# Kernel optimization log

Measured on AMD Instinct MI355X. Metric: run time of the kernel, lower is better.

## Reference

```python
import jax, jax.numpy as jnp
import numpy as np

N_NODES = 100000
N_EDGES = 3200000
D_IN = 128
D_OUT = 128
LN_EPS = 1e-5


def setup_inputs() -> dict:
    key = jax.random.key(0)
    k1, k2, k3, k4 = jax.random.split(key, 4)
    x = jax.random.normal(k1, (N_NODES, D_IN), dtype=jnp.float32)
    edge_index = jax.random.randint(k2, (2, N_EDGES), 0, N_NODES, dtype=jnp.int64)
    # GCNConv weight (glorot-ish scale) and bias
    W = jax.random.normal(k3, (D_IN, D_OUT), dtype=jnp.float32) / np.sqrt(D_IN)
    b = jnp.zeros((D_OUT,), dtype=jnp.float32)
    # LayerNorm params
    gamma = jnp.ones((D_OUT,), dtype=jnp.float32)
    beta = jnp.zeros((D_OUT,), dtype=jnp.float32)
    return {"x": x, "edge_index": edge_index, "W": W, "b": b, "gamma": gamma, "beta": beta}


def reference(x, edge_index, W, b, gamma, beta):
    # GCNConv: add self-loops, symmetric degree normalization, aggregate, add bias.
    N = x.shape[0]
    self_loops = jnp.arange(N, dtype=edge_index.dtype)
    row = jnp.concatenate([edge_index[0], self_loops])  # destination
    col = jnp.concatenate([edge_index[1], self_loops])  # source
    deg = jax.ops.segment_sum(jnp.ones(row.shape[0], x.dtype), row, num_segments=N)
    dinv = jnp.where(deg > 0, jax.lax.rsqrt(deg), 0.0)
    norm = dinv[row] * dinv[col]                         # [E+N]
    xw = x @ W                                           # [N, D_OUT]
    msg = norm[:, None] * xw[col]                        # gather + scale [E+N, D_OUT]
    agg = jax.ops.segment_sum(msg, row, num_segments=N) + b  # scatter-add
    # LayerNorm over feature dim
    mu = jnp.mean(agg, axis=-1, keepdims=True)
    var = jnp.mean(jnp.square(agg - mu), axis=-1, keepdims=True)
    h = (agg - mu) * jax.lax.rsqrt(var + LN_EPS) * gamma + beta
    # ReLU; Dropout is identity in eval mode
    return jax.nn.relu(h)
```

## Files before the change

kernel.cpp:

```cpp
#include <hip/hip_runtime.h>

#define N_NODES 100000
#define N_EDGES 3200000
#define D 128
#define NB 782
#define BCAP 5120
#define STAGE 16

typedef __attribute__((ext_vector_type(8))) short bf16x8;
typedef __attribute__((ext_vector_type(4))) float f32x4;

__device__ __forceinline__ float bf2f(unsigned short u) {
  return __uint_as_float(((unsigned)u) << 16);
}
__device__ __forceinline__ unsigned short f2bf(float f) {
  unsigned u = __float_as_uint(f);
  u += 0x7FFF + ((u >> 16) & 1);
  return (unsigned short)(u >> 16);
}

__global__ void detect_kernel(const int* __restrict__ ei32, int* __restrict__ flag) {
  __shared__ int anynz;
  if (threadIdx.x == 0) anynz = 0;
  __syncthreads();
  int v = 0;
  for (int i = threadIdx.x; i < 2048; i += 256) v |= ei32[2 * i + 1];
  if (v) atomicOr(&anynz, 1);
  __syncthreads();
  if (threadIdx.x == 0) *flag = (anynz == 0) ? 1 : 0;
}

__global__ void zero_kernel(int* __restrict__ p, int n) {
  int i = blockIdx.x * blockDim.x + threadIdx.x;
  if (i < n) p[i] = 0;
}

__global__ void prep_w_kernel(const float* __restrict__ W, unsigned short* __restrict__ wTg) {
  int t = threadIdx.x;
  int c = t >> 1, h = t & 1;
  for (int k0 = h * 64; k0 < h * 64 + 64; k0 += 8) {
    unsigned short tmp[8];
#pragma unroll
    for (int j = 0; j < 8; j++) tmp[j] = f2bf(W[(k0 + j) * D + c]);
    *(uint4*)(wTg + c * D + k0) = *(uint4*)tmp;
  }
}

__global__ __launch_bounds__(256) void partition_kernel(const void* __restrict__ edges,
                                                        const int* __restrict__ flag,
                                                        int* __restrict__ gcur,
                                                        unsigned int* __restrict__ bstore) {
  __shared__ unsigned int stage[NB][STAGE];
  __shared__ int scnt[NB];
  const bool is64 = (*flag != 0);
  for (int i = threadIdx.x; i < NB; i += 256) scnt[i] = 0;
  __syncthreads();
  int gstride = gridDim.x * blockDim.x;
  for (int base = blockIdx.x * blockDim.x; base < N_EDGES; base += gstride) {
    int e = base + threadIdx.x;
    if (e < N_EDGES) {
      int r, c;
      if (is64) {
        r = (int)((const long long*)edges)[e];
        c = (int)((const long long*)edges)[N_EDGES + e];
      } else {
        r = ((const int*)edges)[e];
        c = ((const int*)edges)[N_EDGES + e];
      }
      int b = r >> 7;
      unsigned ent = ((unsigned)(r & 127) << 17) | (unsigned)c;
      int pos = atomicAdd(&scnt[b], 1);
      if (pos < STAGE) {
        stage[b][pos] = ent;
      } else {
        int gp = atomicAdd(&gcur[b], 1);
        if (gp < BCAP) bstore[(size_t)b * BCAP + gp] = ent;
      }
    }
    __syncthreads();
    for (int b = threadIdx.x; b < NB; b += 256) {
      if (scnt[b] >= STAGE) {
        int gp = atomicAdd(&gcur[b], STAGE);
        if (gp + STAGE <= BCAP) {
          uint4* dst = (uint4*)&bstore[(size_t)b * BCAP + gp];
          uint4* src = (uint4*)&stage[b][0];
          dst[0] = src[0];
          dst[1] = src[1];
          dst[2] = src[2];
          dst[3] = src[3];
        } else {
          for (int k = 0; k < STAGE; k++)
            if (gp + k < BCAP) bstore[(size_t)b * BCAP + gp + k] = stage[b][k];
        }
        scnt[b] = 0;
      }
    }
    __syncthreads();
  }
  for (int b = threadIdx.x; b < NB; b += 256) {
    int n = scnt[b];
    if (n > STAGE) n = STAGE;
    if (n > 0) {
      int gp = atomicAdd(&gcur[b], n);
      for (int k = 0; k < n; k++)
        if (gp + k < BCAP) bstore[(size_t)b * BCAP + gp + k] = stage[b][k];
    }
  }
}

__global__ __launch_bounds__(256) void bucket_kernel(const int* __restrict__ gcur,
                                                     unsigned int* __restrict__ bstore,
                                                     int* __restrict__ cnt,
                                                     int* __restrict__ start,
                                                     float* __restrict__ dinv) {
  __shared__ unsigned int ent[BCAP];
  __shared__ int lcnt[128];
  __shared__ int s[128];
  __shared__ int loffs[128];
  int b = blockIdx.x, tid = threadIdx.x;
  size_t base = (size_t)b * BCAP;
  int m = gcur[b];
  if (m > BCAP) m = BCAP;
  int nodes = N_NODES - b * 128;
  if (nodes > 128) nodes = 128;

  for (int i = tid; i < m; i += 256) ent[i] = bstore[base + i];
  if (tid < 128) lcnt[tid] = 0;
  __syncthreads();
  for (int i = tid; i < m; i += 256) atomicAdd(&lcnt[ent[i] >> 17], 1);
  __syncthreads();
  if (tid < 128) s[tid] = lcnt[tid];
  __syncthreads();
#pragma unroll
  for (int off = 1; off < 128; off <<= 1) {
    int v = (tid < 128 && tid >= off) ? s[tid - off] : 0;
    __syncthreads();
    if (tid < 128) s[tid] += v;
    __syncthreads();
  }
  if (tid < nodes) {
    int st = (tid == 0) ? 0 : s[tid - 1];
    int node = b * 128 + tid;
    start[node] = (int)base + st;
    cnt[node] = lcnt[tid];
    dinv[node] = rsqrtf((float)(lcnt[tid] + 1));
    loffs[tid] = st;
  }
  __syncthreads();
  for (int i = tid; i < m; i += 256) {
    unsigned u = ent[i];
    int lr = u >> 17;
    int pos = atomicAdd(&loffs[lr], 1);
    bstore[base + pos] = u & 0x1FFFF;
  }
}

__global__ __launch_bounds__(256) void gemm_mfma_kernel(const float* __restrict__ x,
                                                        const unsigned short* __restrict__ wTg,
                                                        const float* __restrict__ dinv,
                                                        unsigned short* __restrict__ y) {
  __shared__ unsigned short xs[64 * 136];
  __shared__ unsigned short wls[128 * 136];
  int tid = threadIdx.x;
  int row0 = blockIdx.x * 64;
  {
    int c = tid >> 1, h = tid & 1;
    const uint4* src = (const uint4*)(wTg + c * D + h * 64);
    uint4* dst = (uint4*)(wls + c * 136 + h * 64);
#pragma unroll
    for (int i = 0; i < 8; i++) dst[i] = src[i];
  }
  {
    int rx = tid >> 2, q = tid & 3;
    int r = row0 + rx;
    if (r > N_NODES - 1) r = N_NODES - 1;
    const float4* src = (const float4*)(x + (size_t)r * D + q * 32);
    uint4* dst = (uint4*)(xs + rx * 136 + q * 32);
#pragma unroll
    for (int i = 0; i < 4; i++) {
      float4 fa = src[2 * i], fb = src[2 * i + 1];
      uint4 p;
      p.x = (unsigned)f2bf(fa.x) | ((unsigned)f2bf(fa.y) << 16);
      p.y = (unsigned)f2bf(fa.z) | ((unsigned)f2bf(fa.w) << 16);
      p.z = (unsigned)f2bf(fb.x) | ((unsigned)f2bf(fb.y) << 16);
      p.w = (unsigned)f2bf(fb.z) | ((unsigned)f2bf(fb.w) << 16);
      dst[i] = p;
    }
  }
  __syncthreads();
  int w = tid >> 6, l = tid & 63;
  int g = l >> 4, ln = l & 15;
  bf16x8 af[4];
#pragma unroll
  for (int kt = 0; kt < 4; kt++)
    af[kt] = *(const bf16x8*)(xs + (w * 16 + ln) * 136 + kt * 32 + g * 8);
  int rbase = row0 + w * 16 + 4 * g;
  float dv[4];
#pragma unroll
  for (int j = 0; j < 4; j++) {
    int r = rbase + j;
    dv[j] = dinv[r < N_NODES ? r : N_NODES - 1];
  }
#pragma unroll
  for (int ct = 0; ct < 8; ct++) {
    f32x4 acc = {0.f, 0.f, 0.f, 0.f};
#pragma unroll
    for (int kt = 0; kt < 4; kt++) {
      bf16x8 bf = *(const bf16x8*)(wls + (ct * 16 + ln) * 136 + kt * 32 + g * 8);
      acc = __builtin_amdgcn_mfma_f32_16x16x32_bf16(af[kt], bf, acc, 0, 0, 0);
    }
#pragma unroll
    for (int j = 0; j < 4; j++) {
      int r = rbase + j;
      if (r < N_NODES) y[(size_t)r * D + ct * 16 + ln] = f2bf(dv[j] * acc[j]);
    }
  }
}

__global__ __launch_bounds__(256) void agg_ln_kernel(
    const unsigned short* __restrict__ y, const unsigned int* __restrict__ csr,
    const int* __restrict__ start, const int* __restrict__ cnt,
    const float* __restrict__ dinv, const float* __restrict__ bias,
    const float* __restrict__ gamma, const float* __restrict__ beta,
    float* __restrict__ out) {
  int wid = threadIdx.x >> 6, lane = threadIdx.x & 63;
  int node = blockIdx.x * 4 + wid;
  if (node >= N_NODES) return;
  int half = lane >> 5, hl = lane & 31;
  int s = start[node];
  int n = cnt[node];
  float a0 = 0.f, a1 = 0.f, a2 = 0.f, a3 = 0.f;
  for (int j = 0; j < n; j += 64) {
    int m = n - j;
    if (m > 64) m = 64;
    int cj = (j + lane < n) ? (int)csr[s + j + lane] : 0;
    int t = 0;
    for (; t + 7 < m; t += 8) {
      int e0 = __shfl(cj, t + half);
      int e1 = __shfl(cj, t + 2 + half);
      int e2 = __shfl(cj, t + 4 + half);
      int e3 = __shfl(cj, t + 6 + half);
      ushort4 v0 = *(const ushort4*)(y + (size_t)e0 * D + hl * 4);
      ushort4 v1 = *(const ushort4*)(y + (size_t)e1 * D + hl * 4);
      ushort4 v2 = *(const ushort4*)(y + (size_t)e2 * D + hl * 4);
      ushort4 v3 = *(const ushort4*)(y + (size_t)e3 * D + hl * 4);
      a0 += bf2f(v0.x) + bf2f(v1.x) + bf2f(v2.x) + bf2f(v3.x);
      a1 += bf2f(v0.y) + bf2f(v1.y) + bf2f(v2.y) + bf2f(v3.y);
      a2 += bf2f(v0.z) + bf2f(v1.z) + bf2f(v2.z) + bf2f(v3.z);
      a3 += bf2f(v0.w) + bf2f(v1.w) + bf2f(v2.w) + bf2f(v3.w);
    }
    for (; t + 1 < m; t += 2) {
      int e0 = __shfl(cj, t + half);
      ushort4 v0 = *(const ushort4*)(y + (size_t)e0 * D + hl * 4);
      a0 += bf2f(v0.x);
      a1 += bf2f(v0.y);
      a2 += bf2f(v0.z);
      a3 += bf2f(v0.w);
    }
    if (t < m) {
      int e0 = __shfl(cj, t);
      if (half == 0) {
        ushort4 v0 = *(const ushort4*)(y + (size_t)e0 * D + hl * 4);
        a0 += bf2f(v0.x);
        a1 += bf2f(v0.y);
        a2 += bf2f(v0.z);
        a3 += bf2f(v0.w);
      }
    }
  }
  a0 += __shfl_xor(a0, 32);
  a1 += __shfl_xor(a1, 32);
  a2 += __shfl_xor(a2, 32);
  a3 += __shfl_xor(a3, 32);
  ushort4 sv = *(const ushort4*)(y + (size_t)node * D + hl * 4);
  a0 += bf2f(sv.x);
  a1 += bf2f(sv.y);
  a2 += bf2f(sv.z);
  a3 += bf2f(sv.w);
  float di = dinv[node];
  float4 bi = *(const float4*)(bias + hl * 4);
  float v0 = fmaf(di, a0, bi.x);
  float v1 = fmaf(di, a1, bi.y);
  float v2 = fmaf(di, a2, bi.z);
  float v3 = fmaf(di, a3, bi.w);
  float sum = v0 + v1 + v2 + v3;
#pragma unroll
  for (int msk = 1; msk <= 32; msk <<= 1) sum += __shfl_xor(sum, msk);
  float mu = sum * (1.0f / 256.0f);
  float d0 = v0 - mu, d1 = v1 - mu, d2 = v2 - mu, d3 = v3 - mu;
  float sq = d0 * d0 + d1 * d1 + d2 * d2 + d3 * d3;
#pragma unroll
  for (int msk = 1; msk <= 32; msk <<= 1) sq += __shfl_xor(sq, msk);
  float rstd = rsqrtf(sq * (1.0f / 256.0f) + 1e-5f);
  float4 ga = *(const float4*)(gamma + hl * 4);
  float4 be = *(const float4*)(beta + hl * 4);
  if (half == 0) {
    float4 o;
    o.x = fmaxf(fmaf(d0 * rstd, ga.x, be.x), 0.0f);
    o.y = fmaxf(fmaf(d1 * rstd, ga.y, be.y), 0.0f);
    o.z = fmaxf(fmaf(d2 * rstd, ga.z, be.z), 0.0f);
    o.w = fmaxf(fmaf(d3 * rstd, ga.w, be.w), 0.0f);
    *(float4*)(out + (size_t)node * D + hl * 4) = o;
  }
}

extern "C" void kernel_launch(void* const* d_in, const int* in_sizes, int n_in,
                              void* d_out, int out_size, void* d_ws, size_t ws_size,
                              hipStream_t stream) {
  const float* x = (const float*)d_in[0];
  const void* edges = d_in[1];
  const float* W = (const float*)d_in[2];
  const float* b = (const float*)d_in[3];
  const float* gamma = (const float*)d_in[4];
  const float* beta = (const float*)d_in[5];
  float* out = (float*)d_out;

  char* w = (char*)d_ws;
  size_t off = 0;
  auto take = [&](size_t bytes) {
    size_t r = off;
    off += (bytes + 255) & ~(size_t)255;
    return r;
  };
  int* flag = (int*)(w + take(256));
  int* gcur = (int*)(w + take((size_t)NB * 4));
  int* cnt = (int*)(w + take((size_t)N_NODES * 4));
  int* start = (int*)(w + take((size_t)N_NODES * 4));
  float* dinv = (float*)(w + take((size_t)N_NODES * 4));
  unsigned short* wTg = (unsigned short*)(w + take((size_t)D * D * 2));
  unsigned int* bstore = (unsigned int*)(w + take((size_t)NB * BCAP * 4));
  unsigned short* y = (unsigned short*)(w + take((size_t)N_NODES * D * 2));

  detect_kernel<<<1, 256, 0, stream>>>((const int*)edges, flag);
  zero_kernel<<<(NB + 255) / 256, 256, 0, stream>>>(gcur, NB);
  prep_w_kernel<<<1, 256, 0, stream>>>(W, wTg);
  partition_kernel<<<768, 256, 0, stream>>>(edges, flag, gcur, bstore);
  bucket_kernel<<<NB, 256, 0, stream>>>(gcur, bstore, cnt, start, dinv);
  gemm_mfma_kernel<<<(N_NODES + 63) / 64, 256, 0, stream>>>(x, wTg, dinv, y);
  agg_ln_kernel<<<(N_NODES + 3) / 4, 256, 0, stream>>>(y, bstore, start, cnt, dinv, b, gamma,
                                                       beta, out);
}
```

Measured before the change: 328.8 us.

## Sub-sort CSR neighbors by source range and widen gather to 16-byte loads

Bucket counting now keys each edge by destination node and the top bits of the source index, so every node's neighbor list comes out roughly sorted by source. The aim is better cache locality when the aggregation kernel gathers rows of y. The aggregation kernel moves from 4 row-groups of 8-byte loads to 4 quarter-wave groups of 16-byte loads with 8 accumulators per lane, which means fewer load instructions per edge. The zero kernel is replaced by hipMemsetAsync. In exchange, the bucket kernel has a larger histogram and a 256-wide scan, and the wider loads raise register pressure in the aggregation kernel.

```diff
diff --git a/kernel.cpp b/kernel.cpp
--- a/kernel.cpp
+++ b/kernel.cpp
@@ -6,6 +6,7 @@
 #define NB 782
 #define BCAP 5120
 #define STAGE 16
+#define NKEY 1024
 
 typedef __attribute__((ext_vector_type(8))) short bf16x8;
 typedef __attribute__((ext_vector_type(4))) float f32x4;
@@ -28,11 +29,6 @@
   if (v) atomicOr(&anynz, 1);
   __syncthreads();
   if (threadIdx.x == 0) *flag = (anynz == 0) ? 1 : 0;
-}
-
-__global__ void zero_kernel(int* __restrict__ p, int n) {
-  int i = blockIdx.x * blockDim.x + threadIdx.x;
-  if (i < n) p[i] = 0;
 }
 
 __global__ void prep_w_kernel(const float* __restrict__ W, unsigned short* __restrict__ wTg) {
@@ -114,9 +110,9 @@
                                                      int* __restrict__ start,
                                                      float* __restrict__ dinv) {
   __shared__ unsigned int ent[BCAP];
-  __shared__ int lcnt[128];
-  __shared__ int s[128];
-  __shared__ int loffs[128];
+  __shared__ int kc[NKEY];
+  __shared__ int koff[NKEY];
+  __shared__ int psum[256];
   int b = blockIdx.x, tid = threadIdx.x;
   size_t base = (size_t)b * BCAP;
   int m = gcur[b];
@@ -125,32 +121,47 @@
   if (nodes > 128) nodes = 128;
 
   for (int i = tid; i < m; i += 256) ent[i] = bstore[base + i];
-  if (tid < 128) lcnt[tid] = 0;
-  __syncthreads();
-  for (int i = tid; i < m; i += 256) atomicAdd(&lcnt[ent[i] >> 17], 1);
-  __syncthreads();
-  if (tid < 128) s[tid] = lcnt[tid];
-  __syncthreads();
-#pragma unroll
-  for (int off = 1; off < 128; off <<= 1) {
-    int v = (tid < 128 && tid >= off) ? s[tid - off] : 0;
+  for (int i = tid; i < NKEY; i += 256) kc[i] = 0;
+  __syncthreads();
+  for (int i = tid; i < m; i += 256) {
+    unsigned u = ent[i];
+    int key = (int)(((u >> 17) << 3) | ((u & 0x1FFFFu) >> 14));
+    atomicAdd(&kc[key], 1);
+  }
+  __syncthreads();
+  int c0 = kc[4 * tid], c1 = kc[4 * tid + 1], c2 = kc[4 * tid + 2], c3 = kc[4 * tid + 3];
+  psum[tid] = c0 + c1 + c2 + c3;
+  __syncthreads();
+#pragma unroll
+  for (int off = 1; off < 256; off <<= 1) {
+    int v = (tid >= off) ? psum[tid - off] : 0;
     __syncthreads();
-    if (tid < 128) s[tid] += v;
+    psum[tid] += v;
     __syncthreads();
   }
+  int o = (tid == 0) ? 0 : psum[tid - 1];
+  kc[4 * tid] = o;
+  kc[4 * tid + 1] = o + c0;
+  kc[4 * tid + 2] = o + c0 + c1;
+  kc[4 * tid + 3] = o + c0 + c1 + c2;
+  koff[4 * tid] = o;
+  koff[4 * tid + 1] = o + c0;
+  koff[4 * tid + 2] = o + c0 + c1;
+  koff[4 * tid + 3] = o + c0 + c1 + c2;
+  __syncthreads();
   if (tid < nodes) {
-    int st = (tid == 0) ? 0 : s[tid - 1];
+    int st = kc[8 * tid];
+    int en = (tid == 127) ? m : kc[8 * (tid + 1)];
     int node = b * 128 + tid;
     start[node] = (int)base + st;
-    cnt[node] = lcnt[tid];
-    dinv[node] = rsqrtf((float)(lcnt[tid] + 1));
-    loffs[tid] = st;
+    cnt[node] = en - st;
+    dinv[node] = rsqrtf((float)(en - st + 1));
   }
   __syncthreads();
   for (int i = tid; i < m; i += 256) {
     unsigned u = ent[i];
-    int lr = u >> 17;
-    int pos = atomicAdd(&loffs[lr], 1);
+    int key = (int)(((u >> 17) << 3) | ((u & 0x1FFFFu) >> 14));
+    int pos = atomicAdd(&koff[key], 1);
     bstore[base + pos] = u & 0x1FFFF;
   }
 }
@@ -226,82 +237,95 @@
   int wid = threadIdx.x >> 6, lane = threadIdx.x & 63;
   int node = blockIdx.x * 4 + wid;
   if (node >= N_NODES) return;
-  int half = lane >> 5, hl = lane & 31;
+  int q = lane >> 4, hl = lane & 15;
   int s = start[node];
   int n = cnt[node];
-  float a0 = 0.f, a1 = 0.f, a2 = 0.f, a3 = 0.f;
+  float a0 = 0.f, a1 = 0.f, a2 = 0.f, a3 = 0.f, a4 = 0.f, a5 = 0.f, a6 = 0.f, a7 = 0.f;
+  const unsigned short* yq = y + hl * 8;
+#define ACC(V)                                       \
+  a0 += __uint_as_float((V).x << 16);                \
+  a1 += __uint_as_float((V).x & 0xFFFF0000u);        \
+  a2 += __uint_as_float((V).y << 16);                \
+  a3 += __uint_as_float((V).y & 0xFFFF0000u);        \
+  a4 += __uint_as_float((V).z << 16);                \
+  a5 += __uint_as_float((V).z & 0xFFFF0000u);        \
+  a6 += __uint_as_float((V).w << 16);                \
+  a7 += __uint_as_float((V).w & 0xFFFF0000u);
   for (int j = 0; j < n; j += 64) {
     int m = n - j;
     if (m > 64) m = 64;
     int cj = (j + lane < n) ? (int)csr[s + j + lane] : 0;
     int t = 0;
-    for (; t + 7 < m; t += 8) {
-      int e0 = __shfl(cj, t + half);
-      int e1 = __shfl(cj, t + 2 + half);
-      int e2 = __shfl(cj, t + 4 + half);
-      int e3 = __shfl(cj, t + 6 + half);
-      ushort4 v0 = *(const ushort4*)(y + (size_t)e0 * D + hl * 4);
-      ushort4 v1 = *(const ushort4*)(y + (size_t)e1 * D + hl * 4);
-      ushort4 v2 = *(const ushort4*)(y + (size_t)e2 * D + hl * 4);
-      ushort4 v3 = *(const ushort4*)(y + (size_t)e3 * D + hl * 4);
-      a0 += bf2f(v0.x) + bf2f(v1.x) + bf2f(v2.x) + bf2f(v3.x);
-      a1 += bf2f(v0.y) + bf2f(v1.y) + bf2f(v2.y) + bf2f(v3.y);
-      a2 += bf2f(v0.z) + bf2f(v1.z) + bf2f(v2.z) + bf2f(v3.z);
-      a3 += bf2f(v0.w) + bf2f(v1.w) + bf2f(v2.w) + bf2f(v3.w);
-    }
-    for (; t + 1 < m; t += 2) {
-      int e0 = __shfl(cj, t + half);
-      ushort4 v0 = *(const ushort4*)(y + (size_t)e0 * D + hl * 4);
-      a0 += bf2f(v0.x);
-      a1 += bf2f(v0.y);
-      a2 += bf2f(v0.z);
-      a3 += bf2f(v0.w);
-    }
-    if (t < m) {
-      int e0 = __shfl(cj, t);
-      if (half == 0) {
-        ushort4 v0 = *(const ushort4*)(y + (size_t)e0 * D + hl * 4);
-        a0 += bf2f(v0.x);
-        a1 += bf2f(v0.y);
-        a2 += bf2f(v0.z);
-        a3 += bf2f(v0.w);
+    for (; t + 15 < m; t += 16) {
+      int e0 = __shfl(cj, t + q);
+      int e1 = __shfl(cj, t + 4 + q);
+      int e2 = __shfl(cj, t + 8 + q);
+      int e3 = __shfl(cj, t + 12 + q);
+      uint4 v0 = *(const uint4*)(yq + (size_t)e0 * D);
+      uint4 v1 = *(const uint4*)(yq + (size_t)e1 * D);
+      uint4 v2 = *(const uint4*)(yq + (size_t)e2 * D);
+      uint4 v3 = *(const uint4*)(yq + (size_t)e3 * D);
+      ACC(v0) ACC(v1) ACC(v2) ACC(v3)
+    }
+    for (; t + 3 < m; t += 4) {
+      int e0 = __shfl(cj, t + q);
+      uint4 v0 = *(const uint4*)(yq + (size_t)e0 * D);
+      ACC(v0)
+    }
+    int rem = m - t;
+    if (rem > 0) {
+      int sl = t + q;
+      if (sl > m - 1) sl = m - 1;
+      int e0 = __shfl(cj, sl);
+      if (q < rem) {
+        uint4 v0 = *(const uint4*)(yq + (size_t)e0 * D);
+        ACC(v0)
       }
     }
   }
-  a0 += __shfl_xor(a0, 32);
-  a1 += __shfl_xor(a1, 32);
-  a2 += __shfl_xor(a2, 32);
-  a3 += __shfl_xor(a3, 32);
-  ushort4 sv = *(const ushort4*)(y + (size_t)node * D + hl * 4);
-  a0 += bf2f(sv.x);
-  a1 += bf2f(sv.y);
-  a2 += bf2f(sv.z);
-  a3 += bf2f(sv.w);
+#define FOLD(A)            \
+  A += __shfl_xor(A, 16);  \
+  A += __shfl_xor(A, 32);
+  FOLD(a0) FOLD(a1) FOLD(a2) FOLD(a3) FOLD(a4) FOLD(a5) FOLD(a6) FOLD(a7)
+  uint4 sv = *(const uint4*)(yq + (size_t)node * D);
+  ACC(sv)
   float di = dinv[node];
-  float4 bi = *(const float4*)(bias + hl * 4);
-  float v0 = fmaf(di, a0, bi.x);
-  float v1 = fmaf(di, a1, bi.y);
-  float v2 = fmaf(di, a2, bi.z);
-  float v3 = fmaf(di, a3, bi.w);
-  float sum = v0 + v1 + v2 + v3;
-#pragma unroll
-  for (int msk = 1; msk <= 32; msk <<= 1) sum += __shfl_xor(sum, msk);
-  float mu = sum * (1.0f / 256.0f);
+  float4 bi0 = *(const float4*)(bias + hl * 8);
+  float4 bi1 = *(const float4*)(bias + hl * 8 + 4);
+  float v0 = fmaf(di, a0, bi0.x), v1 = fmaf(di, a1, bi0.y);
+  float v2 = fmaf(di, a2, bi0.z), v3 = fmaf(di, a3, bi0.w);
+  float v4 = fmaf(di, a4, bi1.x), v5 = fmaf(di, a5, bi1.y);
+  float v6 = fmaf(di, a6, bi1.z), v7 = fmaf(di, a7, bi1.w);
+  float sum = ((v0 + v1) + (v2 + v3)) + ((v4 + v5) + (v6 + v7));
+#pragma unroll
+  for (int msk = 1; msk <= 8; msk <<= 1) sum += __shfl_xor(sum, msk);
+  float mu = sum * (1.0f / 128.0f);
   float d0 = v0 - mu, d1 = v1 - mu, d2 = v2 - mu, d3 = v3 - mu;
-  float sq = d0 * d0 + d1 * d1 + d2 * d2 + d3 * d3;
-#pragma unroll
-  for (int msk = 1; msk <= 32; msk <<= 1) sq += __shfl_xor(sq, msk);
-  float rstd = rsqrtf(sq * (1.0f / 256.0f) + 1e-5f);
-  float4 ga = *(const float4*)(gamma + hl * 4);
-  float4 be = *(const float4*)(beta + hl * 4);
-  if (half == 0) {
-    float4 o;
-    o.x = fmaxf(fmaf(d0 * rstd, ga.x, be.x), 0.0f);
-    o.y = fmaxf(fmaf(d1 * rstd, ga.y, be.y), 0.0f);
-    o.z = fmaxf(fmaf(d2 * rstd, ga.z, be.z), 0.0f);
-    o.w = fmaxf(fmaf(d3 * rstd, ga.w, be.w), 0.0f);
-    *(float4*)(out + (size_t)node * D + hl * 4) = o;
-  }
+  float d4 = v4 - mu, d5 = v5 - mu, d6 = v6 - mu, d7 = v7 - mu;
+  float sq = ((d0 * d0 + d1 * d1) + (d2 * d2 + d3 * d3)) +
+             ((d4 * d4 + d5 * d5) + (d6 * d6 + d7 * d7));
+#pragma unroll
+  for (int msk = 1; msk <= 8; msk <<= 1) sq += __shfl_xor(sq, msk);
+  float rstd = rsqrtf(sq * (1.0f / 128.0f) + 1e-5f);
+  if (q == 0) {
+    float4 ga0 = *(const float4*)(gamma + hl * 8);
+    float4 ga1 = *(const float4*)(gamma + hl * 8 + 4);
+    float4 be0 = *(const float4*)(beta + hl * 8);
+    float4 be1 = *(const float4*)(beta + hl * 8 + 4);
+    float4 o0, o1;
+    o0.x = fmaxf(fmaf(d0 * rstd, ga0.x, be0.x), 0.0f);
+    o0.y = fmaxf(fmaf(d1 * rstd, ga0.y, be0.y), 0.0f);
+    o0.z = fmaxf(fmaf(d2 * rstd, ga0.z, be0.z), 0.0f);
+    o0.w = fmaxf(fmaf(d3 * rstd, ga0.w, be0.w), 0.0f);
+    o1.x = fmaxf(fmaf(d4 * rstd, ga1.x, be1.x), 0.0f);
+    o1.y = fmaxf(fmaf(d5 * rstd, ga1.y, be1.y), 0.0f);
+    o1.z = fmaxf(fmaf(d6 * rstd, ga1.z, be1.z), 0.0f);
+    o1.w = fmaxf(fmaf(d7 * rstd, ga1.w, be1.w), 0.0f);
+    *(float4*)(out + (size_t)node * D + hl * 8) = o0;
+    *(float4*)(out + (size_t)node * D + hl * 8 + 4) = o1;
+  }
+#undef ACC
+#undef FOLD
 }
 
 extern "C" void kernel_launch(void* const* d_in, const int* in_sizes, int n_in,
@@ -332,7 +356,7 @@
   unsigned short* y = (unsigned short*)(w + take((size_t)N_NODES * D * 2));
 
   detect_kernel<<<1, 256, 0, stream>>>((const int*)edges, flag);
-  zero_kernel<<<(NB + 255) / 256, 256, 0, stream>>>(gcur, NB);
+  hipMemsetAsync(gcur, 0, (size_t)NB * 4, stream);
   prep_w_kernel<<<1, 256, 0, stream>>>(W, wTg);
   partition_kernel<<<768, 256, 0, stream>>>(edges, flag, gcur, bstore);
   bucket_kernel<<<NB, 256, 0, stream>>>(gcur, bstore, cnt, start, dinv);
```

After: 328.7 us. No clear change (-0.0%).
